# Optimization experiments

Hardware: AMD Instinct MI355X
Metric: run time of the kernel (lower is better)

## Reference

```python
import jax, jax.numpy as jnp
import numpy as np

B, FIN, V, X, Y, Z = 2, 32, 768, 8, 8, 8
K, FOUT = 5, 32
NNZ = V * 8  # ~8 neighbors per vertex


def setup_inputs() -> dict:
    key = jax.random.key(0)
    k1, k2, k3, k4, k5 = jax.random.split(key, 5)
    std = np.sqrt(2.0 / (FIN * K)).astype(np.float32)
    return {
        "lap_rows": jax.random.randint(k1, (NNZ,), 0, V, dtype=jnp.int32),
        "lap_cols": jax.random.randint(k2, (NNZ,), 0, V, dtype=jnp.int32),
        "lap_vals": jax.random.normal(k3, (NNZ,), dtype=jnp.float32) * 0.1,
        "x": jax.random.normal(k4, (B, FIN, V, X, Y, Z), dtype=jnp.float32),
        "weight": jax.random.normal(k5, (K, FIN, FOUT), dtype=jnp.float32) * std,
        "bias": jnp.full((FOUT,), 0.01, dtype=jnp.float32),
    }


def reference(lap_rows, lap_cols, lap_vals, x, weight, bias):
    Bb, Fin, Vv, Xx, Yy, Zz = x.shape
    Kk, _, Fout = weight.shape

    def spmm(v):  # sparse [V,V] @ dense [V,D]
        return jax.ops.segment_sum(lap_vals[:, None] * v[lap_cols],
                                   lap_rows, num_segments=Vv)

    # [B,Fin,V,X,Y,Z] -> [V, Fin*B*X*Y*Z]
    x0 = jnp.transpose(x, (2, 1, 0, 3, 4, 5)).reshape(Vv, -1)
    xs = [x0]
    if Kk > 1:
        x1 = spmm(x0)
        xs.append(x1)
        for _ in range(2, Kk):
            x2 = 2.0 * spmm(x1) - x0
            xs.append(x2)
            x0, x1 = x1, x2
    basis = jnp.stack(xs, axis=0)  # [K, V, Fin*B*X*Y*Z]
    basis = basis.reshape(Kk, Vv, Fin, Bb, Xx, Yy, Zz)
    basis = jnp.transpose(basis, (3, 1, 4, 5, 6, 0, 2))  # [B,V,X,Y,Z,K,Fin]
    out = basis.reshape(-1, Kk * Fin) @ weight.reshape(Kk * Fin, Fout)
    out = out.reshape(Bb, Vv, Xx, Yy, Zz, Fout)
    out = jnp.transpose(out, (0, 5, 1, 2, 3, 4))  # [B,Fout,V,X,Y,Z]
    return out + bias[None, :, None, None, None, None]
```

## Files before the change

kernel.cpp:

```cpp
#include <hip/hip_runtime.h>
#include <stdint.h>

#define V      768
#define FINC   32
#define FOUTC  32
#define XYZ    512
#define NB     2
#define ROWP   40
#define QROW   48
#define MAXDEG 32
#define EROWS  36

typedef unsigned short u16;
typedef unsigned int   u32;
typedef short bf16x8 __attribute__((ext_vector_type(8)));
typedef float f32x4  __attribute__((ext_vector_type(4)));
typedef float f32x2  __attribute__((ext_vector_type(2)));

__device__ __forceinline__ u16 f2bf(float f) {
  u32 u = __float_as_uint(f);
  u32 r = u + 0x7fffu + ((u >> 16) & 1u);
  return (u16)(r >> 16);
}
__device__ __forceinline__ float bflo(u32 w) { return __uint_as_float(w << 16); }
__device__ __forceinline__ float bfhi(u32 w) { return __uint_as_float(w & 0xffff0000u); }
__device__ __forceinline__ u32 cvtpk_bf16(float lo, float hi) {
  u32 r;
  asm("v_cvt_pk_bf16_f32 %0, %1, %2" : "=v"(r) : "v"(lo), "v"(hi));
  return r;
}

__global__ __launch_bounds__(64) void build_ell(const int* __restrict__ rows,
                                                const int* __restrict__ cols,
                                                const float* __restrict__ vals,
                                                int nnz,
                                                int2* __restrict__ epair,
                                                int* __restrict__ deg) {
  int v = blockIdx.x;
  int lane = threadIdx.x;
  int cnt = 0;
  for (int base = 0; base < nnz; base += 64) {
    int i = base + lane;
    bool m = (i < nnz) && (rows[i] == v);
    unsigned long long mask = __ballot(m);
    if (m) {
      int pos = cnt + __popcll(mask & ((1ull << lane) - 1ull));
      if (pos < MAXDEG)
        epair[v * MAXDEG + pos] = make_int2(cols[i], __float_as_int(vals[i]));
    }
    cnt += __popcll(mask);
  }
  int d = cnt < MAXDEG ? cnt : MAXDEG;
  for (int p = d + lane; p < MAXDEG; p += 64)
    epair[v * MAXDEG + p] = make_int2(0, 0);
  if (lane == 0) deg[v] = d;
}

__global__ __launch_bounds__(V) void sort_rows(const int* __restrict__ deg,
                                               int* __restrict__ perm,
                                               int* __restrict__ inv_g,
                                               int* __restrict__ wtrip) {
  __shared__ int sdeg[V];
  int v = threadIdx.x;
  int d = deg[v];
  sdeg[v] = d;
  __syncthreads();
  int r = 0;
  for (int u = 0; u < V; ++u) {
    int du = sdeg[u];
    r += (du > d) || (du == d && u < v);
  }
  const unsigned long long GPK = 0x8495A6B73210ull;
  int w = (int)((GPK >> (4 * (r >> 6))) & 15ull);
  int p = w * 64 + (r & 63);
  perm[p] = v;
  inv_g[v] = p;
  if ((r & 63) == 0) wtrip[w] = d;
}

#define TXV 12
__global__ __launch_bounds__(512) void transpose_x(const float* __restrict__ x,
                                                   const int* __restrict__ perm,
                                                   const int* __restrict__ deg,
                                                   const int2* __restrict__ epair,
                                                   const int* __restrict__ inv_g,
                                                   int2* __restrict__ ep3,
                                                   u16* __restrict__ xT) {
  __shared__ u32 TL2[384 * 34];
  __shared__ int PV[TXV];
  int g = blockIdx.x;
  int t = threadIdx.x;
  if (g < EROWS) {
    int e = g;
    for (int p = t; p < V; p += 512) {
      int v = perm[p];
      int d = deg[v];
      int2 o = make_int2(0, 0);
      if (e < d) {
        int2 pe = epair[v * MAXDEG + e];
        o = make_int2(inv_g[pe.x] * QROW, pe.y);
      }
      ep3[e * V + p] = o;
    }
  }
  int b = g >> 9, pvt = (g >> 3) & 63, xt = g & 7;
  int pv0 = pvt * TXV;
  int xyz0 = xt * 64;
  if (t < TXV) PV[t] = perm[pv0 + t];
  __syncthreads();
  int q = t & 15;
  int rgrp = t >> 4;
#pragma unroll
  for (int st = 0; st < 12; ++st) {
    int row = st * 32 + rgrp;
    int vloc = row >> 5, f = row & 31;
    const float4 xv = *(const float4*)&x[((size_t)(b * FINC + f) * V + PV[vloc]) * XYZ + xyz0 + 4 * q];
    u32 A = cvtpk_bf16(xv.x, xv.y);
    u32 B = cvtpk_bf16(xv.z, xv.w);
    *(uint2*)&TL2[row * 34 + 2 * q] = make_uint2(A, B);
  }
  __syncthreads();
  const u16* TL16 = (const u16*)TL2;
  int s = t & 7, xyz = t >> 3;
  u32* dst = (u32*)(xT + ((size_t)(b * XYZ + xyz0 + xyz) * V + pv0) * FINC);
#pragma unroll
  for (int it = 0; it < 24; ++it) {
    int i = s + 8 * it;
    u32 lo = TL16[(2 * i) * 68 + xyz];
    u32 hi = TL16[(2 * i + 1) * 68 + xyz];
    dst[i] = lo | (hi << 16);
  }
}

__global__ __launch_bounds__(1024, 4) void cheb_main(
    const u16* __restrict__ xT, const int2* __restrict__ ep3,
    const int* __restrict__ perm, const int* __restrict__ wtrip,
    const float* __restrict__ weight, const float* __restrict__ bias,
    u32* __restrict__ stage) {
  __shared__ __align__(16) u16   CUR[V * ROWP];
  __shared__ __align__(16) unsigned char CURQ[V * QROW];
  __shared__ __align__(16) uint4 WF[5][2][64];
  __shared__ u16 PRM[V];
  __shared__ int WT[12];

  int g = blockIdx.x;
  int xcd = g & 7;
  int u = g >> 3;
  int phase = u >> 5;
  int xyz = xcd * 32 + (u & 31) + (phase & 1) * 256;
  int b = phase >> 1;
  int slice = b * XYZ + xyz;

  int tid = threadIdx.x;
  int lane = tid & 63;
  int w = tid >> 6;
  int l15 = lane & 15, l4 = lane >> 4;
  bool gath = tid < V;

  if (tid < 640) {
    int k = tid >> 7, n = (tid >> 6) & 1, ln = tid & 63;
    int a15 = ln & 15, a4 = ln >> 4;
    u32 pw[4];
#pragma unroll
    for (int p = 0; p < 4; ++p) {
      float w0 = weight[(size_t)(k * FINC + a4 * 8 + 2 * p) * FOUTC + n * 16 + a15];
      float w1 = weight[(size_t)(k * FINC + a4 * 8 + 2 * p + 1) * FOUTC + n * 16 + a15];
      pw[p] = (u32)f2bf(w0) | ((u32)f2bf(w1) << 16);
    }
    WF[k][n][ln] = make_uint4(pw[0], pw[1], pw[2], pw[3]);
  }
  if (tid < 12) WT[tid] = wtrip[tid];
  if (gath) PRM[tid] = (u16)perm[tid];
  float bsv[2] = {bias[l15], bias[16 + l15]};

  if (gath) {
    const uint4* src = (const uint4*)(xT + (size_t)slice * V * FINC) + tid * 4;
    uint4* dst = (uint4*)(CUR + tid * ROWP);
    u32 cw[16], q8[8];
#pragma unroll
    for (int j = 0; j < 4; ++j) {
      uint4 q = src[j];
      dst[j] = q;
      cw[4 * j] = q.x; cw[4 * j + 1] = q.y;
      cw[4 * j + 2] = q.z; cw[4 * j + 3] = q.w;
    }
#pragma unroll
    for (int d = 0; d < 8; ++d) {
      u32 p0 = cw[2 * d], p1 = cw[2 * d + 1];
      u32 q = __builtin_amdgcn_cvt_pk_fp8_f32(bflo(p0), bfhi(p0), 0, false);
      q8[d] = __builtin_amdgcn_cvt_pk_fp8_f32(bflo(p1), bfhi(p1), q, true);
    }
    uint4* qp = (uint4*)(CURQ + tid * QROW);
    qp[0] = make_uint4(q8[0], q8[1], q8[2], q8[3]);
    qp[1] = make_uint4(q8[4], q8[5], q8[6], q8[7]);
  }
  __syncthreads();

  int trip = 0;
  if (w < 12) trip = __builtin_amdgcn_readfirstlane(WT[w]);
  const int2* pp = ep3 + tid;

  f32x4 acc[3][2];
#pragma unroll
  for (int a = 0; a < 3; ++a)
#pragma unroll
    for (int n = 0; n < 2; ++n) acc[a][n] = (f32x4){0.f, 0.f, 0.f, 0.f};

  auto gemm_acc = [&](int k) {
    bf16x8 bn0 = *(const bf16x8*)&WF[k][0][lane];
    bf16x8 bn1 = *(const bf16x8*)&WF[k][1][lane];
#pragma unroll
    for (int a = 0; a < 3; ++a) {
      int row = w * 48 + a * 16 + l15;
      bf16x8 af = *(const bf16x8*)(CUR + row * ROWP + l4 * 8);
      acc[a][0] = __builtin_amdgcn_mfma_f32_16x16x32_bf16(af, bn0, acc[a][0], 0, 0, 0);
      acc[a][1] = __builtin_amdgcn_mfma_f32_16x16x32_bf16(af, bn1, acc[a][1], 0, 0, 0);
    }
  };

  f32x2 fa2[16];
  auto fma_edge8 = [&](float fv, uint4 qa, uint4 qb) {
    f32x2 fv2 = {fv, fv};
    u32 wq[8] = {qa.x, qa.y, qa.z, qa.w, qb.x, qb.y, qb.z, qb.w};
#pragma unroll
    for (int d = 0; d < 8; ++d) {
      f32x2 s0 = __builtin_amdgcn_cvt_pk_f32_fp8(wq[d], false);
      f32x2 s1 = __builtin_amdgcn_cvt_pk_f32_fp8(wq[d], true);
      fa2[2 * d]     += fv2 * s0;
      fa2[2 * d + 1] += fv2 * s1;
    }
  };
  auto gather = [&]() {
#pragma unroll
    for (int j = 0; j < 16; ++j) fa2[j] = (f32x2){0.f, 0.f};
    int trips = (trip + 1) & ~1;
    int2 r0 = pp[0], r1 = pp[V], r2 = pp[2 * V];
    const uint4* s0 = (const uint4*)(CURQ + (u32)r0.x);
    uint4 A0 = s0[0], A1 = s0[1];
    for (int e = 0; e < trips; e += 2) {
      const uint4* s1 = (const uint4*)(CURQ + (u32)r1.x);
      uint4 B0 = s1[0], B1 = s1[1];
      int2 n3 = pp[(e + 3) * V];
      fma_edge8(__int_as_float(r0.y), A0, A1);
      const uint4* s2 = (const uint4*)(CURQ + (u32)r2.x);
      A0 = s2[0]; A1 = s2[1];
      int2 n4 = pp[(e + 4) * V];
      fma_edge8(__int_as_float(r1.y), B0, B1);
      r0 = r2; r1 = n3; r2 = n4;
    }
  };

  u32 prevpk[16];

#pragma unroll
  for (int ph = 0; ph <= 3; ++ph) {
    gemm_acc(ph);
    if (gath) gather();
    __syncthreads();
    if (gath) {
      uint4* cp = (uint4*)(CUR + tid * ROWP);
      uint4 c0 = cp[0], c1 = cp[1], c2 = cp[2], c3 = cp[3];
      u32 cw[16] = {c0.x, c0.y, c0.z, c0.w, c1.x, c1.y, c1.z, c1.w,
                    c2.x, c2.y, c2.z, c2.w, c3.x, c3.y, c3.z, c3.w};
      u32 npk[16], q8[8];
      if (ph == 0) {
#pragma unroll
        for (int j = 0; j < 16; ++j) {
          float t0 = fa2[j][0], t1 = fa2[j][1];
          npk[j] = cvtpk_bf16(t0, t1);
          if ((j & 1) == 0) q8[j >> 1] = __builtin_amdgcn_cvt_pk_fp8_f32(t0, t1, 0, false);
          else              q8[j >> 1] = __builtin_amdgcn_cvt_pk_fp8_f32(t0, t1, q8[j >> 1], true);
        }
      } else {
#pragma unroll
        for (int j = 0; j < 16; ++j) {
          u32 pv = prevpk[j];
          float t0 = 2.f * fa2[j][0] - bflo(pv);
          float t1 = 2.f * fa2[j][1] - bfhi(pv);
          npk[j] = cvtpk_bf16(t0, t1);
          if ((j & 1) == 0) q8[j >> 1] = __builtin_amdgcn_cvt_pk_fp8_f32(t0, t1, 0, false);
          else              q8[j >> 1] = __builtin_amdgcn_cvt_pk_fp8_f32(t0, t1, q8[j >> 1], true);
        }
      }
#pragma unroll
      for (int j = 0; j < 16; ++j) prevpk[j] = cw[j];
      cp[0] = make_uint4(npk[0], npk[1], npk[2], npk[3]);
      cp[1] = make_uint4(npk[4], npk[5], npk[6], npk[7]);
      cp[2] = make_uint4(npk[8], npk[9], npk[10], npk[11]);
      cp[3] = make_uint4(npk[12], npk[13], npk[14], npk[15]);
      uint4* qp = (uint4*)(CURQ + tid * QROW);
      qp[0] = make_uint4(q8[0], q8[1], q8[2], q8[3]);
      qp[1] = make_uint4(q8[4], q8[5], q8[6], q8[7]);
    }
    __syncthreads();
  }

  gemm_acc(4);

  u32* stg = stage + (size_t)slice * (V * 16);
#pragma unroll
  for (int a = 0; a < 3; ++a) {
#pragma unroll
    for (int r = 0; r < 4; ++r) {
      int vr = PRM[w * 48 + a * 16 + l4 * 4 + r];
      u32 pk = cvtpk_bf16(acc[a][0][r] + bsv[0], acc[a][1][r] + bsv[1]);
      stg[vr * 16 + l15] = pk;
    }
  }
}

#define TO_VT  12
#define TO_PAD 193
__global__ __launch_bounds__(512) void transpose_out(const u32* __restrict__ stage,
                                                     float* __restrict__ out) {
  __shared__ u32 T[64 * TO_PAD];
  int g = blockIdx.x;
  int b = g >> 9, vt = (g >> 3) & 63, xt = g & 7;
  int v0 = vt * TO_VT;
  int xyz0 = xt * 64;
  int t = threadIdx.x;
  const u32* base = stage + (size_t)(b * XYZ + xyz0) * (V * 16) + v0 * 16;
#pragma unroll
  for (int i = 0; i < 6; ++i) {
    int idx4 = i * 512 + t;
    int j = idx4 / 48;
    int c4 = idx4 - j * 48;
    uint4 q = *(const uint4*)(base + (size_t)j * (V * 16) + c4 * 4);
    int w0 = c4 * 4;
    T[j * TO_PAD + w0]     = q.x;
    T[j * TO_PAD + w0 + 1] = q.y;
    T[j * TO_PAD + w0 + 2] = q.z;
    T[j * TO_PAD + w0 + 3] = q.w;
  }
  __syncthreads();
  int xyz2 = t & 31;
  int grp = t >> 5;
#pragma unroll
  for (int i = 0; i < 24; ++i) {
    int fout = grp * 2 + (i & 1);
    int vv = i >> 1;
    int col = vv * 16 + (fout & 15);
    u32 pka = T[(2 * xyz2) * TO_PAD + col];
    u32 pkb = T[(2 * xyz2 + 1) * TO_PAD + col];
    float va = (fout < 16) ? bflo(pka) : bfhi(pka);
    float vb = (fout < 16) ? bflo(pkb) : bfhi(pkb);
    *(float2*)&out[((size_t)(b * FOUTC + fout) * V + v0 + vv) * XYZ + xyz0 + 2 * xyz2] =
        make_float2(va, vb);
  }
}

extern "C" void kernel_launch(void* const* d_in, const int* in_sizes, int n_in,
                              void* d_out, int out_size, void* d_ws, size_t ws_size,
                              hipStream_t stream) {
  const int*   lap_rows = (const int*)d_in[0];
  const int*   lap_cols = (const int*)d_in[1];
  const float* lap_vals = (const float*)d_in[2];
  const float* x        = (const float*)d_in[3];
  const float* weight   = (const float*)d_in[4];
  const float* bias     = (const float*)d_in[5];
  float* out = (float*)d_out;
  int nnz = in_sizes[0];

  char* ws = (char*)d_ws;
  const size_t XT_BYTES = (size_t)NB * XYZ * V * FINC * sizeof(u16);
  const size_t EP_BYTES = (size_t)V * MAXDEG * 8;
  const size_t E3_BYTES = (size_t)EROWS * V * 8;
  u16*  xT    = (u16*)ws;
  u32*  stg   = (u32*)ws;
  int2* epair = (int2*)(ws + XT_BYTES);
  int2* ep3   = (int2*)(ws + XT_BYTES + EP_BYTES);
  int*  deg   = (int*)(ws + XT_BYTES + EP_BYTES + E3_BYTES);
  int*  perm  = (int*)(ws + XT_BYTES + EP_BYTES + E3_BYTES + 3072);
  int*  inv_g = (int*)(ws + XT_BYTES + EP_BYTES + E3_BYTES + 6144);
  int*  wtrip = (int*)(ws + XT_BYTES + EP_BYTES + E3_BYTES + 9216);

  hipLaunchKernelGGL(build_ell, dim3(V), dim3(64), 0, stream,
                     lap_rows, lap_cols, lap_vals, nnz, epair, deg);
  hipLaunchKernelGGL(sort_rows, dim3(1), dim3(V), 0, stream,
                     deg, perm, inv_g, wtrip);
  hipLaunchKernelGGL(transpose_x, dim3(NB * 64 * 8), dim3(512), 0, stream,
                     x, perm, deg, epair, inv_g, ep3, xT);
  hipLaunchKernelGGL(cheb_main, dim3(NB * XYZ), dim3(1024), 0, stream,
                     xT, ep3, perm, wtrip, weight, bias, stg);
  hipLaunchKernelGGL(transpose_out, dim3(NB * 64 * 8), dim3(512), 0, stream,
                     stg, out);
}
```

Measured before the change: 182.2 us.

## Merge ELL build and sort into one prep kernel, fold ELL fill into transpose

Replaces the separate build_ell and sort_rows launches with a single-block prep kernel. That kernel computes row degrees with a shared-memory atomic histogram, zeroes ep3 and ranks the rows. The per-row ELL gather, which writes ep3 directly in permuted order, now runs inside transpose_x for the first V blocks. This removes one launch and the intermediate epair/deg buffers. The cost is a serial 768-step rank loop in one block and extra work in some transpose blocks; ordering within a row depends on the ballot scan, the same as before.

```diff
diff --git a/kernel.cpp b/kernel.cpp
--- a/kernel.cpp
+++ b/kernel.cpp
@@ -30,79 +30,51 @@
   return r;
 }
 
-__global__ __launch_bounds__(64) void build_ell(const int* __restrict__ rows,
-                                                const int* __restrict__ cols,
-                                                const float* __restrict__ vals,
-                                                int nnz,
-                                                int2* __restrict__ epair,
-                                                int* __restrict__ deg) {
-  int v = blockIdx.x;
-  int lane = threadIdx.x;
-  int cnt = 0;
-  for (int base = 0; base < nnz; base += 64) {
-    int i = base + lane;
-    bool m = (i < nnz) && (rows[i] == v);
-    unsigned long long mask = __ballot(m);
-    if (m) {
-      int pos = cnt + __popcll(mask & ((1ull << lane) - 1ull));
-      if (pos < MAXDEG)
-        epair[v * MAXDEG + pos] = make_int2(cols[i], __float_as_int(vals[i]));
-    }
-    cnt += __popcll(mask);
-  }
-  int d = cnt < MAXDEG ? cnt : MAXDEG;
-  for (int p = d + lane; p < MAXDEG; p += 64)
-    epair[v * MAXDEG + p] = make_int2(0, 0);
-  if (lane == 0) deg[v] = d;
-}
-
-__global__ __launch_bounds__(V) void sort_rows(const int* __restrict__ deg,
-                                               int* __restrict__ perm,
-                                               int* __restrict__ inv_g,
-                                               int* __restrict__ wtrip) {
-  __shared__ int sdeg[V];
-  int v = threadIdx.x;
-  int d = deg[v];
-  sdeg[v] = d;
-  __syncthreads();
-  int r = 0;
-  for (int u = 0; u < V; ++u) {
-    int du = sdeg[u];
-    r += (du > d) || (du == d && u < v);
-  }
-  const unsigned long long GPK = 0x8495A6B73210ull;
-  int w = (int)((GPK >> (4 * (r >> 6))) & 15ull);
-  int p = w * 64 + (r & 63);
-  perm[p] = v;
-  inv_g[v] = p;
-  if ((r & 63) == 0) wtrip[w] = d;
+__global__ __launch_bounds__(1024) void prep(const int* __restrict__ rows, int nnz,
+                                             int* __restrict__ perm,
+                                             int* __restrict__ inv_g,
+                                             int* __restrict__ wtrip,
+                                             int2* __restrict__ ep3) {
+  __shared__ int hist[V];
+  int t = threadIdx.x;
+  if (t < V) hist[t] = 0;
+  __syncthreads();
+  for (int i = t; i < nnz; i += 1024)
+    atomicAdd(&hist[rows[i]], 1);
+  __syncthreads();
+  if (t < V) hist[t] = hist[t] < MAXDEG ? hist[t] : MAXDEG;
+  for (int i = t; i < EROWS * V; i += 1024) ep3[i] = make_int2(0, 0);
+  __syncthreads();
+  if (t < V) {
+    int d = hist[t];
+    int r = 0;
+    for (int u = 0; u < V; ++u) {
+      int du = hist[u];
+      r += (du > d) || (du == d && u < t);
+    }
+    const unsigned long long GPK = 0x8495A6B73210ull;
+    int w = (int)((GPK >> (4 * (r >> 6))) & 15ull);
+    int p = w * 64 + (r & 63);
+    perm[p] = t;
+    inv_g[t] = p;
+    if ((r & 63) == 0) wtrip[w] = d;
+  }
 }
 
 #define TXV 12
 __global__ __launch_bounds__(512) void transpose_x(const float* __restrict__ x,
                                                    const int* __restrict__ perm,
-                                                   const int* __restrict__ deg,
-                                                   const int2* __restrict__ epair,
                                                    const int* __restrict__ inv_g,
+                                                   const int* __restrict__ rows,
+                                                   const int* __restrict__ cols,
+                                                   const float* __restrict__ vals,
+                                                   int nnz,
                                                    int2* __restrict__ ep3,
                                                    u16* __restrict__ xT) {
   __shared__ u32 TL2[384 * 34];
   __shared__ int PV[TXV];
   int g = blockIdx.x;
   int t = threadIdx.x;
-  if (g < EROWS) {
-    int e = g;
-    for (int p = t; p < V; p += 512) {
-      int v = perm[p];
-      int d = deg[v];
-      int2 o = make_int2(0, 0);
-      if (e < d) {
-        int2 pe = epair[v * MAXDEG + e];
-        o = make_int2(inv_g[pe.x] * QROW, pe.y);
-      }
-      ep3[e * V + p] = o;
-    }
-  }
   int b = g >> 9, pvt = (g >> 3) & 63, xt = g & 7;
   int pv0 = pvt * TXV;
   int xyz0 = xt * 64;
@@ -129,6 +101,23 @@
     u32 lo = TL16[(2 * i) * 68 + xyz];
     u32 hi = TL16[(2 * i + 1) * 68 + xyz];
     dst[i] = lo | (hi << 16);
+  }
+  if (g < V && t < 64) {
+    int v = g;
+    int p = inv_g[v];
+    int lane = t;
+    int cnt = 0;
+    for (int base = 0; base < nnz; base += 64) {
+      int i = base + lane;
+      bool m = (i < nnz) && (rows[i] == v);
+      unsigned long long mask = __ballot(m);
+      if (m) {
+        int pos = cnt + __popcll(mask & ((1ull << lane) - 1ull));
+        if (pos < MAXDEG)
+          ep3[pos * V + p] = make_int2(inv_g[cols[i]] * QROW, __float_as_int(vals[i]));
+      }
+      cnt += __popcll(mask);
+    }
   }
 }
 
@@ -363,23 +352,18 @@
 
   char* ws = (char*)d_ws;
   const size_t XT_BYTES = (size_t)NB * XYZ * V * FINC * sizeof(u16);
-  const size_t EP_BYTES = (size_t)V * MAXDEG * 8;
   const size_t E3_BYTES = (size_t)EROWS * V * 8;
   u16*  xT    = (u16*)ws;
   u32*  stg   = (u32*)ws;
-  int2* epair = (int2*)(ws + XT_BYTES);
-  int2* ep3   = (int2*)(ws + XT_BYTES + EP_BYTES);
-  int*  deg   = (int*)(ws + XT_BYTES + EP_BYTES + E3_BYTES);
-  int*  perm  = (int*)(ws + XT_BYTES + EP_BYTES + E3_BYTES + 3072);
-  int*  inv_g = (int*)(ws + XT_BYTES + EP_BYTES + E3_BYTES + 6144);
-  int*  wtrip = (int*)(ws + XT_BYTES + EP_BYTES + E3_BYTES + 9216);
-
-  hipLaunchKernelGGL(build_ell, dim3(V), dim3(64), 0, stream,
-                     lap_rows, lap_cols, lap_vals, nnz, epair, deg);
-  hipLaunchKernelGGL(sort_rows, dim3(1), dim3(V), 0, stream,
-                     deg, perm, inv_g, wtrip);
+  int2* ep3   = (int2*)(ws + XT_BYTES);
+  int*  perm  = (int*)(ws + XT_BYTES + E3_BYTES);
+  int*  inv_g = (int*)(ws + XT_BYTES + E3_BYTES + 3072);
+  int*  wtrip = (int*)(ws + XT_BYTES + E3_BYTES + 6144);
+
+  hipLaunchKernelGGL(prep, dim3(1), dim3(1024), 0, stream,
+                     lap_rows, nnz, perm, inv_g, wtrip, ep3);
   hipLaunchKernelGGL(transpose_x, dim3(NB * 64 * 8), dim3(512), 0, stream,
-                     x, perm, deg, epair, inv_g, ep3, xT);
+                     x, perm, inv_g, lap_rows, lap_cols, lap_vals, nnz, ep3, xT);
   hipLaunchKernelGGL(cheb_main, dim3(NB * XYZ), dim3(1024), 0, stream,
                      xT, ep3, perm, wtrip, weight, bias, stg);
   hipLaunchKernelGGL(transpose_out, dim3(NB * 64 * 8), dim3(512), 0, stream,
```

After: 181.3 us. Within noise of the previous version (-0.5%).
